# Kernel tuning notes

Measured on AMD Instinct MI355X. Metric: run time of the kernel, lower is better.

The kernel has to match this reference:

```python
import jax, jax.numpy as jnp
import numpy as np


def setup_inputs() -> dict:
    key = jax.random.key(0)
    k1, k2, k3, k4, k5 = jax.random.split(key, 5)
    B, C, H, W = 8, 32, 64, 64
    inp = jax.random.normal(k1, (B, C, H, W), dtype=jnp.float32)
    # expected positions lie inside the image grid
    exPx = jax.random.uniform(k2, (B, H, W), dtype=jnp.float32) * (W - 1)
    exPy = jax.random.uniform(k3, (B, H, W), dtype=jnp.float32) * (H - 1)
    # positive Gaussian widths in roughly [1, 3]
    sigmax = jax.random.uniform(k4, (B, H, W), dtype=jnp.float32) * 2.0 + 1.0
    sigmay = jax.random.uniform(k5, (B, H, W), dtype=jnp.float32) * 2.0 + 1.0
    return {"input": inp, "exPx": exPx, "exPy": exPy,
            "sigmax": sigmax, "sigmay": sigmay}


def reference(input, exPx, exPy, sigmax, sigmay):
    """Gaussian-weighted spatial swap/warp (soft gather).

    For each output pixel (i, j):
      out[b,c,i,j] = sum_{u,v} G(u; exPy[b,i,j], sigmay[b,i,j])
                              * G(v; exPx[b,i,j], sigmax[b,i,j])
                              * input[b,c,u,v]  /  Z[b,i,j]
    where G is an unnormalized Gaussian and Z is the total weight mass.
    The 2D Gaussian weight is separable, so we contract rows then cols.
    """
    B, C, H, W = input.shape
    u = jnp.arange(H, dtype=input.dtype)  # source row coords (y)
    v = jnp.arange(W, dtype=input.dtype)  # source col coords (x)
    # wy: [B,H,W,H] weight over source rows u for each output pixel (i,j)
    wy = jnp.exp(-0.5 * ((u[None, None, None, :] - exPy[..., None]) / sigmay[..., None]) ** 2)
    # wx: [B,H,W,W] weight over source cols v
    wx = jnp.exp(-0.5 * ((v[None, None, None, :] - exPx[..., None]) / sigmax[..., None]) ** 2)
    # normalization mass per output pixel
    Z = wy.sum(-1) * wx.sum(-1) + jnp.asarray(1e-8, input.dtype)  # [B,H,W]
    # contract over source rows u -> [B,C,H,W,W]
    t = jnp.einsum('biju,bcuv->bcijv', wy, input)
    # contract over source cols v -> [B,C,H,W]
    out = jnp.einsum('bcijv,bijv->bcij', t, wx)
    return out / Z[:, None]
```

## Files before the change

### kernel.cpp

```cpp
#include <hip/hip_runtime.h>


#define BB 8
#define CC 32
#define HH 64
#define WW 64

typedef __attribute__((ext_vector_type(8))) short short8;
typedef __attribute__((ext_vector_type(4))) float f32x4;
typedef unsigned int uint;

__device__ __forceinline__ uint rn_bf16(float f) {
    uint u = __float_as_uint(f);
    return (u + 0x7FFFu + ((u >> 16) & 1u)) >> 16;
}

__global__ void preconvert_kernel(const float* __restrict__ x, uint* __restrict__ hi)
{
    const int n = BB * CC * HH * WW / 2;
    int idx = blockIdx.x * blockDim.x + threadIdx.x;
    for (; idx < n; idx += gridDim.x * blockDim.x) {
        const float2 d = ((const float2*)x)[idx];
        hi[idx] = rn_bf16(d.x) | (rn_bf16(d.y) << 16);
    }
}

#define WYS_OFF   0
#define WXH_OFF   16896
#define SUM_OFF   26112
#define INVZ_OFF  28160
#define LDS_BYTES 28416

__global__ __launch_bounds__(256, 2)
void swap_mfma_kernel(const uint* __restrict__ xhi,
                      const float* __restrict__ exPx, const float* __restrict__ exPy,
                      const float* __restrict__ sigmax, const float* __restrict__ sigmay,
                      float* __restrict__ out)
{
    __shared__ __align__(16) char lds[LDS_BYTES];
    const int t    = threadIdx.x;
    const int lane = t & 63;
    const int w    = t >> 6;
    const int q    = (t >> 4) & 3;
    const int ln   = t & 15;
    const int bid  = blockIdx.x;
    const int b    = bid & 7;
    const int i    = bid >> 3;
    const int bi   = b * 64 + i;

    const int cplane0 = b * CC + w * 8;
    const uint* xbase = xhi + (size_t)cplane0 * 2048 + ln * 32 + q * 4;
    union AU { uint4 v; short8 s; };
    AU abuf[2][4][2];
    #pragma unroll
    for (int cc = 0; cc < 2; ++cc)
        #pragma unroll
        for (int mt = 0; mt < 4; ++mt) {
            abuf[cc][mt][0].v = *(const uint4*)(xbase + cc * 2048 + mt * 512);
            abuf[cc][mt][1].v = *(const uint4*)(xbase + cc * 2048 + mt * 512 + 16);
        }

    float* WYS = (float*)(lds + WYS_OFF);

    {
        const int p = lane;
        const int g = w;
        const int pixBase = bi * 64 + p;
        const float ey = exPy[pixBase], ex = exPx[pixBase];
        const float isy = 1.0f / sigmay[pixBase], isx = 1.0f / sigmax[pixBase];
        float sy = 0.0f, sx = 0.0f;
        #pragma unroll
        for (int k = 0; k < 16; ++k) {
            const int u = g * 16 + k;
            const float dy = ((float)u - ey) * isy;
            const float wy = __expf(-0.5f * dy * dy);
            WYS[u * 66 + p] = wy;
            sy += wy;
        }
        uint* WXH = (uint*)(lds + WXH_OFF);
        #pragma unroll
        for (int j = 0; j < 8; ++j) {
            const int v0 = g * 16 + 2 * j;
            const float dx0 = ((float)v0       - ex) * isx;
            const float dx1 = ((float)(v0 + 1) - ex) * isx;
            const float wx0 = __expf(-0.5f * dx0 * dx0);
            const float wx1 = __expf(-0.5f * dx1 * dx1);
            sx += wx0 + wx1;
            WXH[p * 36 + g * 8 + j] = rn_bf16(wx0) | (rn_bf16(wx1) << 16);
        }
        float* SUMY = (float*)(lds + SUM_OFF);
        float* SUMX = SUMY + 256;
        SUMY[g * 64 + p] = sy;
        SUMX[g * 64 + p] = sx;
    }
    __syncthreads();
    float* INVZ = (float*)(lds + INVZ_OFF);
    if (t < 64) {
        float* SUMY = (float*)(lds + SUM_OFF);
        float* SUMX = SUMY + 256;
        const float sy = SUMY[t] + SUMY[64 + t] + SUMY[128 + t] + SUMY[192 + t];
        const float sx = SUMX[t] + SUMX[64 + t] + SUMX[128 + t] + SUMX[192 + t];
        INVZ[t] = 1.0f / (sy * sx + 1e-8f);
    }
    __syncthreads();

    short8 bh[4][2];
    #pragma unroll
    for (int nt = 0; nt < 4; ++nt)
        #pragma unroll
        for (int ks = 0; ks < 2; ++ks)
            bh[nt][ks] = *(const short8*)(lds + WXH_OFF + (nt * 16 + ln) * 144 + ks * 64 + q * 16);
    float wyz[4][4][4];
    #pragma unroll
    for (int nt = 0; nt < 4; ++nt) {
        const float iz = INVZ[nt * 16 + ln];
        #pragma unroll
        for (int mt = 0; mt < 4; ++mt)
            #pragma unroll
            for (int rr = 0; rr < 4; ++rr)
                wyz[mt][nt][rr] = WYS[(mt * 16 + q * 4 + rr) * 66 + nt * 16 + ln] * iz;
    }

    float* obase = out + (size_t)cplane0 * 4096 + i * 64 + lane;

    #pragma unroll
    for (int c = 0; c < 8; ++c) {
        float ps[4] = {0.f, 0.f, 0.f, 0.f};
        #pragma unroll
        for (int mt = 0; mt < 4; ++mt) {
            f32x4 acc[4];
            #pragma unroll
            for (int nt = 0; nt < 4; ++nt) acc[nt] = (f32x4){0.f, 0.f, 0.f, 0.f};
            #pragma unroll
            for (int nt = 0; nt < 4; ++nt) {
                acc[nt] = __builtin_amdgcn_mfma_f32_16x16x32_bf16(abuf[c & 1][mt][0].s, bh[nt][0], acc[nt], 0, 0, 0);
                acc[nt] = __builtin_amdgcn_mfma_f32_16x16x32_bf16(abuf[c & 1][mt][1].s, bh[nt][1], acc[nt], 0, 0, 0);
            }
            #pragma unroll
            for (int nt = 0; nt < 4; ++nt)
                ps[nt] += acc[nt][0] * wyz[mt][nt][0] + acc[nt][1] * wyz[mt][nt][1]
                        + acc[nt][2] * wyz[mt][nt][2] + acc[nt][3] * wyz[mt][nt][3];
        }
        if (c + 2 < 8) {
            const uint* xn = xbase + (c + 2) * 2048;
            #pragma unroll
            for (int mt = 0; mt < 4; ++mt) {
                abuf[c & 1][mt][0].v = *(const uint4*)(xn + mt * 512);
                abuf[c & 1][mt][1].v = *(const uint4*)(xn + mt * 512 + 16);
            }
        }
        #pragma unroll
        for (int nt = 0; nt < 4; ++nt) {
            ps[nt] += __shfl_xor(ps[nt], 16, 64);
            ps[nt] += __shfl_xor(ps[nt], 32, 64);
        }
        const float po = (q == 0) ? ps[0] : (q == 1) ? ps[1] : (q == 2) ? ps[2] : ps[3];
        obase[(size_t)c * 4096] = po;
    }
}

__device__ __forceinline__ void split_pair(float f0, float f1, uint& hi, uint& lo) {
    const uint u0 = __float_as_uint(f0), u1 = __float_as_uint(f1);
    hi = (u0 >> 16) | (u1 & 0xFFFF0000u);
    const float l0 = f0 - __uint_as_float(u0 & 0xFFFF0000u);
    const float l1 = f1 - __uint_as_float(u1 & 0xFFFF0000u);
    lo = (__float_as_uint(l0) >> 16) | (__float_as_uint(l1) & 0xFFFF0000u);
}

#define FB_WYS_OFF   0
#define FB_WXH_OFF   16640
#define FB_SUM_OFF   25856
#define FB_INVZ_OFF  27904
#define FB_LDS_BYTES 28160
#define FB_RED_OFF   0

__global__ __launch_bounds__(256, 4)
void swap_fused_kernel(const float* __restrict__ inp,
                       const float* __restrict__ exPx, const float* __restrict__ exPy,
                       const float* __restrict__ sigmax, const float* __restrict__ sigmay,
                       float* __restrict__ out)
{
    __shared__ __align__(16) char lds[FB_LDS_BYTES];
    const int t = threadIdx.x;
    const int lane = t & 63, w = t >> 6, q = (t >> 4) & 3, ln = t & 15;
    const int bid = blockIdx.x;
    const int b = bid & 7, r = bid >> 3;
    const int chalf = r & 1, i = r >> 1;
    const int bi = b * 64 + i;

    float* WYS = (float*)(lds + FB_WYS_OFF);
    {
        const int p = lane, g = w;
        const int pixBase = bi * 64 + p;
        const float ey = exPy[pixBase], ex = exPx[pixBase];
        const float isy = 1.0f / sigmay[pixBase], isx = 1.0f / sigmax[pixBase];
        float sy = 0.0f, sx = 0.0f;
        #pragma unroll
        for (int k = 0; k < 16; ++k) {
            const int u = g * 16 + k;
            const float dy = ((float)u - ey) * isy;
            const float wy = __expf(-0.5f * dy * dy);
            WYS[u * 65 + p] = wy; sy += wy;
        }
        uint* WXH = (uint*)(lds + FB_WXH_OFF);
        #pragma unroll
        for (int j = 0; j < 8; ++j) {
            const int v0 = g * 16 + 2 * j;
            const float dx0 = ((float)v0 - ex) * isx;
            const float dx1 = ((float)(v0 + 1) - ex) * isx;
            const float wx0 = __expf(-0.5f * dx0 * dx0);
            const float wx1 = __expf(-0.5f * dx1 * dx1);
            sx += wx0 + wx1;
            WXH[p * 36 + g * 8 + j] = rn_bf16(wx0) | (rn_bf16(wx1) << 16);
        }
        float* SUMY = (float*)(lds + FB_SUM_OFF);
        float* SUMX = SUMY + 256;
        SUMY[g * 64 + p] = sy; SUMX[g * 64 + p] = sx;
    }
    __syncthreads();
    float* INVZ = (float*)(lds + FB_INVZ_OFF);
    if (t < 64) {
        float* SUMY = (float*)(lds + FB_SUM_OFF);
        float* SUMX = SUMY + 256;
        const float sy = SUMY[t] + SUMY[64 + t] + SUMY[128 + t] + SUMY[192 + t];
        const float sx = SUMX[t] + SUMX[64 + t] + SUMX[128 + t] + SUMX[192 + t];
        INVZ[t] = 1.0f / (sy * sx + 1e-8f);
    }
    __syncthreads();
    short8 bh[4][2];
    #pragma unroll
    for (int nt = 0; nt < 4; ++nt)
        #pragma unroll
        for (int ks = 0; ks < 2; ++ks)
            bh[nt][ks] = *(const short8*)(lds + FB_WXH_OFF + (nt * 16 + ln) * 144 + ks * 64 + q * 16);
    float wyz[4][4];
    #pragma unroll
    for (int nt = 0; nt < 4; ++nt) {
        const float iz = INVZ[nt * 16 + ln];
        #pragma unroll
        for (int rr = 0; rr < 4; ++rr)
            wyz[nt][rr] = WYS[(w * 16 + q * 4 + rr) * 65 + nt * 16 + ln] * iz;
    }
    __syncthreads();
    const int cbase = b * CC + chalf * 16;
    float* RED = (float*)(lds + FB_RED_OFF);
    const float* xrow = inp + (size_t)cbase * 4096 + (w * 16 + ln) * 64 + q * 8;
    #pragma unroll 2
    for (int c = 0; c < 16; ++c) {
        const float4* src = (const float4*)(xrow + (size_t)c * 4096);
        const float4 x0 = src[0], x1 = src[1], x2 = src[8], x3 = src[9];
        union { uint u[4]; short8 s; } Ah0, Al0, Ah1, Al1;
        split_pair(x0.x, x0.y, Ah0.u[0], Al0.u[0]);
        split_pair(x0.z, x0.w, Ah0.u[1], Al0.u[1]);
        split_pair(x1.x, x1.y, Ah0.u[2], Al0.u[2]);
        split_pair(x1.z, x1.w, Ah0.u[3], Al0.u[3]);
        split_pair(x2.x, x2.y, Ah1.u[0], Al1.u[0]);
        split_pair(x2.z, x2.w, Ah1.u[1], Al1.u[1]);
        split_pair(x3.x, x3.y, Ah1.u[2], Al1.u[2]);
        split_pair(x3.z, x3.w, Ah1.u[3], Al1.u[3]);
        f32x4 acc[4];
        #pragma unroll
        for (int nt = 0; nt < 4; ++nt) acc[nt] = (f32x4){0.f, 0.f, 0.f, 0.f};
        #pragma unroll
        for (int nt = 0; nt < 4; ++nt) {
            acc[nt] = __builtin_amdgcn_mfma_f32_16x16x32_bf16(Ah0.s, bh[nt][0], acc[nt], 0, 0, 0);
            acc[nt] = __builtin_amdgcn_mfma_f32_16x16x32_bf16(Al0.s, bh[nt][0], acc[nt], 0, 0, 0);
            acc[nt] = __builtin_amdgcn_mfma_f32_16x16x32_bf16(Ah1.s, bh[nt][1], acc[nt], 0, 0, 0);
            acc[nt] = __builtin_amdgcn_mfma_f32_16x16x32_bf16(Al1.s, bh[nt][1], acc[nt], 0, 0, 0);
        }
        #pragma unroll
        for (int nt = 0; nt < 4; ++nt) {
            float ps = acc[nt][0] * wyz[nt][0] + acc[nt][1] * wyz[nt][1]
                     + acc[nt][2] * wyz[nt][2] + acc[nt][3] * wyz[nt][3];
            ps += __shfl_xor(ps, 16, 64);
            ps += __shfl_xor(ps, 32, 64);
            if (q == 0) RED[c * 256 + w * 64 + nt * 16 + ln] = ps;
        }
    }
    __syncthreads();
    {
        const int kk = t >> 6, p = t & 63;
        #pragma unroll
        for (int g = 0; g < 4; ++g) {
            const int c = g * 4 + kk;
            const float* Rk = RED + c * 256;
            const float o = Rk[p] + Rk[64 + p] + Rk[128 + p] + Rk[192 + p];
            out[(size_t)(cbase + c) * (HH * WW) + i * 64 + p] = o;
        }
    }
}

extern "C" void kernel_launch(void* const* d_in, const int* in_sizes, int n_in,
                              void* d_out, int out_size, void* d_ws, size_t ws_size,
                              hipStream_t stream) {
    const float* inp    = (const float*)d_in[0];
    const float* exPx   = (const float*)d_in[1];
    const float* exPy   = (const float*)d_in[2];
    const float* sigmax = (const float*)d_in[3];
    const float* sigmay = (const float*)d_in[4];
    float* out = (float*)d_out;

    const size_t plane_bytes = (size_t)BB * CC * HH * WW * 2;
    if (ws_size >= plane_bytes) {
        uint* xhi = (uint*)d_ws;
        hipLaunchKernelGGL(preconvert_kernel, dim3(1024), dim3(256), 0, stream, inp, xhi);
        hipLaunchKernelGGL(swap_mfma_kernel, dim3(BB * HH), dim3(256), 0, stream,
                           xhi, exPx, exPy, sigmax, sigmay, out);
    } else {
        hipLaunchKernelGGL(swap_fused_kernel, dim3(BB * HH * 2), dim3(256), 0, stream,
                           inp, exPx, exPy, sigmax, sigmay, out);
    }
}
```

Baseline: 80.53 us.

## Merge bf16 preconversion and MFMA swap into one cooperative kernel with grid sync

Folds the fp32-to-bf16 preconversion pass into the main MFMA kernel using a cooperative launch with a grid-wide barrier between the two phases. Each of the 512 blocks converts a strided slice of the input, synchronizes across the grid, then runs the unchanged swap body. The aim is to remove one kernel launch and the gap between kernels. In exchange it adds a grid-sync cost and requires all 512 blocks to be co-resident; if the cooperative launch fails it falls back to the two-kernel path.

```diff
diff --git a/kernel.cpp b/kernel.cpp
--- a/kernel.cpp
+++ b/kernel.cpp
@@ -1,4 +1,5 @@
 #include <hip/hip_runtime.h>
+#include <hip/hip_cooperative_groups.h>
 
 
 #define BB 8
@@ -31,13 +32,12 @@
 #define INVZ_OFF  28160
 #define LDS_BYTES 28416
 
-__global__ __launch_bounds__(256, 2)
-void swap_mfma_kernel(const uint* __restrict__ xhi,
-                      const float* __restrict__ exPx, const float* __restrict__ exPy,
-                      const float* __restrict__ sigmax, const float* __restrict__ sigmay,
-                      float* __restrict__ out)
-{
-    __shared__ __align__(16) char lds[LDS_BYTES];
+__device__ __forceinline__
+void swap_body(const uint* __restrict__ xhi,
+               const float* __restrict__ exPx, const float* __restrict__ exPy,
+               const float* __restrict__ sigmax, const float* __restrict__ sigmay,
+               float* __restrict__ out, char* lds)
+{
     const int t    = threadIdx.x;
     const int lane = t & 63;
     const int w    = t >> 6;
@@ -157,6 +157,37 @@
         const float po = (q == 0) ? ps[0] : (q == 1) ? ps[1] : (q == 2) ? ps[2] : ps[3];
         obase[(size_t)c * 4096] = po;
     }
+}
+
+__global__ __launch_bounds__(256, 2)
+void swap_coop_kernel(const float* __restrict__ inp, uint* __restrict__ xhi,
+                      const float* __restrict__ exPx, const float* __restrict__ exPy,
+                      const float* __restrict__ sigmax, const float* __restrict__ sigmay,
+                      float* __restrict__ out)
+{
+    __shared__ __align__(16) char lds[LDS_BYTES];
+    {
+        const int gtid = blockIdx.x * 256 + threadIdx.x;
+        const float2* src = (const float2*)inp;
+        #pragma unroll
+        for (int k = 0; k < 4; ++k) {
+            const int idx = gtid + k * 131072;
+            const float2 d = src[idx];
+            xhi[idx] = rn_bf16(d.x) | (rn_bf16(d.y) << 16);
+        }
+    }
+    cooperative_groups::this_grid().sync();
+    swap_body(xhi, exPx, exPy, sigmax, sigmay, out, lds);
+}
+
+__global__ __launch_bounds__(256, 2)
+void swap_mfma_kernel(const uint* __restrict__ xhi,
+                      const float* __restrict__ exPx, const float* __restrict__ exPy,
+                      const float* __restrict__ sigmax, const float* __restrict__ sigmay,
+                      float* __restrict__ out)
+{
+    __shared__ __align__(16) char lds[LDS_BYTES];
+    swap_body(xhi, exPx, exPy, sigmax, sigmay, out, lds);
 }
 
 __device__ __forceinline__ void split_pair(float f0, float f1, uint& hi, uint& lo) {
@@ -303,9 +334,16 @@
     const size_t plane_bytes = (size_t)BB * CC * HH * WW * 2;
     if (ws_size >= plane_bytes) {
         uint* xhi = (uint*)d_ws;
-        hipLaunchKernelGGL(preconvert_kernel, dim3(1024), dim3(256), 0, stream, inp, xhi);
-        hipLaunchKernelGGL(swap_mfma_kernel, dim3(BB * HH), dim3(256), 0, stream,
-                           xhi, exPx, exPy, sigmax, sigmay, out);
+        void* args[] = {(void*)&inp, (void*)&xhi, (void*)&exPx, (void*)&exPy,
+                        (void*)&sigmax, (void*)&sigmay, (void*)&out};
+        hipError_t e = hipLaunchCooperativeKernel((const void*)swap_coop_kernel,
+                                                  dim3(BB * HH), dim3(256),
+                                                  args, 0, stream);
+        if (e != hipSuccess) {
+            hipLaunchKernelGGL(preconvert_kernel, dim3(1024), dim3(256), 0, stream, inp, xhi);
+            hipLaunchKernelGGL(swap_mfma_kernel, dim3(BB * HH), dim3(256), 0, stream,
+                               xhi, exPx, exPy, sigmax, sigmay, out);
+        }
     } else {
         hipLaunchKernelGGL(swap_fused_kernel, dim3(BB * HH * 2), dim3(256), 0, stream,
                            inp, exPx, exPy, sigmax, sigmay, out);
```

Measured after the change: 160.2 us. 1.99x slower.
